# Kernel optimization log

Measured on AMD Instinct MI355X. Metric: run time of the kernel, lower is better.

The kernel has to match this reference:

```python
import jax, jax.numpy as jnp
import numpy as np

B, CIN, COUT, H, W, WDIM = 16, 256, 256, 64, 64, 512


def setup_inputs() -> dict:
    key = jax.random.key(0)
    ks = jax.random.split(key, 4)
    return {
        "x": jax.random.normal(ks[0], (B, CIN, H, W), dtype=jnp.float32),
        "w": jax.random.normal(ks[1], (B, WDIM), dtype=jnp.float32),
        "affine_w": jax.random.normal(ks[2], (CIN, WDIM), dtype=jnp.float32),
        "affine_b": jnp.ones((CIN,), dtype=jnp.float32),
        "weight": jax.random.normal(ks[3], (COUT, CIN, 1, 1), dtype=jnp.float32),
        "bias": jnp.zeros((COUT,), dtype=jnp.float32),
    }


def reference(x, w, affine_w, affine_b, weight, bias):
    # Affine: FullyConnectedLayer with weight_gain = 1/sqrt(w_dim), bias_init=1
    wg = 1.0 / np.sqrt(WDIM).astype(np.float32)
    styles = w @ (affine_w.T * wg) + affine_b  # [B, CIN]

    # Pre-normalize weight and styles (demodulate branch)
    wk = weight[:, :, 0, 0]  # [COUT, CIN] (1x1 kernel)
    wk = wk * jax.lax.rsqrt(jnp.mean(jnp.square(weight), axis=(1, 2, 3)))[:, None]
    s = styles * jax.lax.rsqrt(jnp.mean(jnp.square(styles)))  # [B, CIN]

    # Per-sample modulated weights: [B, COUT, CIN]
    wb = wk[None, :, :] * s[:, None, :]
    dcoef = jax.lax.rsqrt(jnp.sum(jnp.square(wb), axis=2) + 1e-8)  # [B, COUT]
    wb = wb * dcoef[:, :, None]

    # Grouped 1x1 conv == batched GEMM over spatial positions
    y = jnp.einsum('bihw,boi->bohw', x, wb) + bias[None, :, None, None]

    # Bilinear upsample x2 (align_corners=False == half-pixel, jax default)
    y = jax.image.resize(y, (B, COUT, 2 * H, 2 * W), method='bilinear')
    return y
```

## Files before the change

### kernel.cpp

```cpp
#include <hip/hip_runtime.h>
#include <hip/hip_bf16.h>

#define B_   16
#define CIN  256
#define COUT 256
#define HH   64
#define WW   64
#define WDIM 512
#define OH   128
#define OW   128

typedef __attribute__((ext_vector_type(8))) short short8;
typedef __attribute__((ext_vector_type(4))) float f32x4;

__device__ __forceinline__ unsigned short f2bf(float f) {
    __hip_bfloat16 h = __float2bfloat16(f);
    return *reinterpret_cast<unsigned short*>(&h);
}
__device__ __forceinline__ float bf2f(unsigned short u) {
    unsigned int t = ((unsigned int)u) << 16;
    return *reinterpret_cast<float*>(&t);
}


__global__ __launch_bounds__(256) void k_styles(const float* __restrict__ w,
                                                const float* __restrict__ aw,
                                                const float* __restrict__ ab,
                                                float* __restrict__ ws) {
    int b = blockIdx.x, i = threadIdx.x;
    const float4* wr = (const float4*)(w + b * WDIM);
    const float4* ar = (const float4*)(aw + (size_t)i * WDIM);
    float acc = 0.f;
    #pragma unroll 4
    for (int k = 0; k < WDIM / 4; ++k) {
        float4 wv = wr[k], av = ar[k];
        acc += wv.x * av.x + wv.y * av.y + wv.z * av.z + wv.w * av.w;
    }
    const float wg = 0.04419417382415922f;
    float st = acc * wg + ab[i];
    ws[64 + b * CIN + i] = st;
    __shared__ float sred[256];
    sred[i] = st * st;
    __syncthreads();
    for (int s = 128; s > 0; s >>= 1) {
        if (i < s) sred[i] += sred[i + s];
        __syncthreads();
    }
    if (i == 0) ws[b] = sred[0];
}

__global__ __launch_bounds__(64) void k_wb(const float* __restrict__ weight,
                                           const float* __restrict__ ws,
                                           unsigned short* __restrict__ wb) {
    int o = blockIdx.x, b = blockIdx.y, l = threadIdx.x;
    float tot = 0.f;
    #pragma unroll
    for (int j = 0; j < B_; ++j) tot += ws[j];
    float srs = rsqrtf(tot / (float)(B_ * CIN));
    float4 wk = *(const float4*)(weight + (size_t)o * CIN + l * 4);
    float ss = wk.x * wk.x + wk.y * wk.y + wk.z * wk.z + wk.w * wk.w;
    #pragma unroll
    for (int off = 32; off; off >>= 1) ss += __shfl_xor(ss, off);
    float wkn = rsqrtf(ss / (float)CIN);
    float4 st = *(const float4*)(ws + 64 + b * CIN + l * 4);
    float4 t;
    t.x = wk.x * wkn * st.x * srs;
    t.y = wk.y * wkn * st.y * srs;
    t.z = wk.z * wkn * st.z * srs;
    t.w = wk.w * wkn * st.w * srs;
    float s2 = t.x * t.x + t.y * t.y + t.z * t.z + t.w * t.w;
    #pragma unroll
    for (int off = 32; off; off >>= 1) s2 += __shfl_xor(s2, off);
    float dcoef = rsqrtf(s2 + 1e-8f);
    ushort4 pk;
    pk.x = f2bf(t.x * dcoef);
    pk.y = f2bf(t.y * dcoef);
    pk.z = f2bf(t.z * dcoef);
    pk.w = f2bf(t.w * dcoef);
    *(ushort4*)(wb + ((size_t)b * COUT + o) * CIN + l * 4) = pk;
}

__global__ __launch_bounds__(512, 4) void k_conv5(const float* __restrict__ x,
                                                  const float* __restrict__ bias,
                                                  const unsigned short* __restrict__ wb,
                                                  unsigned short* __restrict__ y) {
    __shared__ __align__(16) unsigned short xt[128 * CIN];
    const int r2 = blockIdx.x * 2;
    const int b = blockIdx.y;
    const int tid = threadIdx.x;
    const int lane = tid & 63;
    const int wv = tid >> 6;
    const int lo = lane & 15, hi = lane >> 4;

    const unsigned short* wbb = wb + (size_t)b * COUT * CIN;
    short8 breg[2][8];
    #pragma unroll
    for (int c = 0; c < 2; ++c) {
        const int m0 = (wv * 2 + c) * 16;
        const unsigned short* wrow = wbb + (size_t)(m0 + lo) * CIN + hi * 8;
        #pragma unroll
        for (int ks = 0; ks < 8; ++ks)
            breg[c][ks] = *(const short8*)(wrow + ks * 32);
    }

    {
        const int c4 = tid & 15;
        const int rowsel = (tid >> 4) & 1;
        const int ig = tid >> 5;
        const float* xp = x + (size_t)b * CIN * (HH * WW) + (size_t)(r2 + rowsel) * WW + c4 * 4;
        const int pxbase = rowsel * 64 + c4 * 4;
        #pragma unroll
        for (int p = 0; p < 8; ++p) {
            const int i0 = ig * 16 + p * 2;
            float4 v0 = *(const float4*)(xp + (size_t)i0 * (HH * WW));
            float4 v1 = *(const float4*)(xp + (size_t)(i0 + 1) * (HH * WW));
            const int ib = i0 >> 3, e = i0 & 7;
            #pragma unroll
            for (int j = 0; j < 4; ++j) {
                const int px = pxbase + j;
                float f0 = (j == 0) ? v0.x : (j == 1) ? v0.y : (j == 2) ? v0.z : v0.w;
                float f1 = (j == 0) ? v1.x : (j == 1) ? v1.y : (j == 2) ? v1.z : v1.w;
                unsigned int pk = (unsigned int)f2bf(f0) | ((unsigned int)f2bf(f1) << 16);
                const int swz = ib ^ (px & 31) ^ ((px >> 2) & 7);
                *(unsigned int*)&xt[px * 256 + (swz << 3) + e] = pk;
            }
        }
    }
    __syncthreads();

    unsigned short* yb = y + (size_t)b * COUT * (HH * WW);

    #pragma unroll
    for (int c = 0; c < 2; ++c) {
        const int m0 = (wv * 2 + c) * 16;
        const float bs = bias[m0 + lo];
        unsigned short* yrow = yb + (size_t)(m0 + lo) * (HH * WW);
        #pragma unroll
        for (int g = 0; g < 8; ++g) {
            f32x4 acc = {0.f, 0.f, 0.f, 0.f};
            #pragma unroll
            for (int ks = 0; ks < 8; ++ks) {
                const int px = g * 16 + lo;
                const int ib = ks * 4 + hi;
                const int swz = ib ^ (px & 31) ^ ((px >> 2) & 7);
                short8 a = *(const short8*)&xt[px * 256 + (swz << 3)];
                acc = __builtin_amdgcn_mfma_f32_16x16x32_bf16(a, breg[c][ks], acc, 0, 0, 0);
            }
            ushort4 pk;
            pk.x = f2bf(acc[0] + bs);
            pk.y = f2bf(acc[1] + bs);
            pk.z = f2bf(acc[2] + bs);
            pk.w = f2bf(acc[3] + bs);
            const int prow = g >> 2;
            const int pcol = (g & 3) * 16 + hi * 4;
            *(ushort4*)(yrow + (size_t)(r2 + prow) * WW + pcol) = pk;
        }
    }
}

__global__ __launch_bounds__(256, 8) void k_up(const unsigned short* __restrict__ y,
                                               float* __restrict__ out) {
    const int tid = threadIdx.x;
    const int t = tid & 31;
    const int s = tid >> 5;
    const int idx = blockIdx.x * 8 + s;
    const int p = idx & 63;
    const int ch = (idx >> 6) & 255;
    const int b = idx >> 14;

    const unsigned short* yb = y + (size_t)(b * COUT + ch) * (HH * WW);
    const int pm1 = max(p - 1, 0), pp1 = min(p + 1, HH - 1);
    unsigned int T  = *(const unsigned int*)(yb + pm1 * WW + 2 * t);
    unsigned int M  = *(const unsigned int*)(yb + p   * WW + 2 * t);
    unsigned int Bt = *(const unsigned int*)(yb + pp1 * WW + 2 * t);

    float tB = bf2f((unsigned short)(T & 0xffff)),  tC = bf2f((unsigned short)(T >> 16));
    float mB = bf2f((unsigned short)(M & 0xffff)),  mC = bf2f((unsigned short)(M >> 16));
    float bB = bf2f((unsigned short)(Bt & 0xffff)), bC = bf2f((unsigned short)(Bt >> 16));

    float aB = 0.25f * tB + 0.75f * mB, aC = 0.25f * tC + 0.75f * mC;
    float eB = 0.75f * mB + 0.25f * bB, eC = 0.75f * mC + 0.25f * bC;

    float aA = __shfl_up(aC, 1, 32);   if (t == 0)  aA = aB;
    float aD = __shfl_down(aB, 1, 32); if (t == 31) aD = aC;
    float eA = __shfl_up(eC, 1, 32);   if (t == 0)  eA = eB;
    float eD = __shfl_down(eB, 1, 32); if (t == 31) eD = eC;

    float4 o0, o1;
    o0.x = 0.25f * aA + 0.75f * aB;
    o0.y = 0.75f * aB + 0.25f * aC;
    o0.z = 0.25f * aB + 0.75f * aC;
    o0.w = 0.75f * aC + 0.25f * aD;
    o1.x = 0.25f * eA + 0.75f * eB;
    o1.y = 0.75f * eB + 0.25f * eC;
    o1.z = 0.25f * eB + 0.75f * eC;
    o1.w = 0.75f * eC + 0.25f * eD;

    float* op = out + (size_t)(b * COUT + ch) * (OH * OW) + (2 * p) * OW + 4 * t;
    *(float4*)op = o0;
    *(float4*)(op + OW) = o1;
}

extern "C" void kernel_launch(void* const* d_in, const int* in_sizes, int n_in,
                              void* d_out, int out_size, void* d_ws, size_t ws_size,
                              hipStream_t stream) {
    (void)in_sizes; (void)n_in; (void)out_size; (void)ws_size;
    const float* x      = (const float*)d_in[0];
    const float* w      = (const float*)d_in[1];
    const float* aw     = (const float*)d_in[2];
    const float* ab     = (const float*)d_in[3];
    const float* weight = (const float*)d_in[4];
    const float* bias   = (const float*)d_in[5];
    float* out = (float*)d_out;
    float* wsf = (float*)d_ws;
    unsigned short* wb = (unsigned short*)((char*)d_ws + 32768);
    unsigned short* y  = (unsigned short*)((char*)d_ws + (4u << 20));

    hipLaunchKernelGGL(k_styles, dim3(16), dim3(256), 0, stream, w, aw, ab, wsf);
    hipLaunchKernelGGL(k_wb, dim3(COUT, B_), dim3(64), 0, stream, weight, wsf, wb);
    hipLaunchKernelGGL(k_conv5, dim3(HH / 2, B_), dim3(512), 0, stream, x, bias, wb, y);
    hipLaunchKernelGGL(k_up, dim3(B_ * COUT * HH / 8), dim3(256), 0, stream, y, out);
}
```

Measured before the change: 111.3 us.

## Fuse 1x1 modulated conv with bilinear upsample using LDS-resident conv output

Merges the conv kernel and the upsample kernel into one kernel. Each block now computes conv output for two adjacent input rows (with halo overlap) into shared memory and writes the upsampled float output directly. This removes the bf16 intermediate write and read through global memory and one kernel launch. In exchange, x loads and conv MFMA work are doubled because neighbouring blocks overlap by one row. LDS use roughly doubles, which lowers occupancy. The second weight register set is also loaded after the barrier to ease register pressure.

Measured after the change: 120.4 us. +8.2%, slower.

```diff
diff --git a/kernel.cpp b/kernel.cpp
--- a/kernel.cpp
+++ b/kernel.cpp
@@ -80,12 +80,13 @@
     *(ushort4*)(wb + ((size_t)b * COUT + o) * CIN + l * 4) = pk;
 }
 
-__global__ __launch_bounds__(512, 4) void k_conv5(const float* __restrict__ x,
+__global__ __launch_bounds__(512, 2) void k_fused(const float* __restrict__ x,
                                                   const float* __restrict__ bias,
                                                   const unsigned short* __restrict__ wb,
-                                                  unsigned short* __restrict__ y) {
+                                                  float* __restrict__ out) {
     __shared__ __align__(16) unsigned short xt[128 * CIN];
-    const int r2 = blockIdx.x * 2;
+    __shared__ __align__(16) unsigned int yl[COUT * 64];
+    const int r = blockIdx.x;
     const int b = blockIdx.y;
     const int tid = threadIdx.x;
     const int lane = tid & 63;
@@ -93,21 +94,21 @@
     const int lo = lane & 15, hi = lane >> 4;
 
     const unsigned short* wbb = wb + (size_t)b * COUT * CIN;
-    short8 breg[2][8];
-    #pragma unroll
-    for (int c = 0; c < 2; ++c) {
-        const int m0 = (wv * 2 + c) * 16;
-        const unsigned short* wrow = wbb + (size_t)(m0 + lo) * CIN + hi * 8;
-        #pragma unroll
-        for (int ks = 0; ks < 8; ++ks)
-            breg[c][ks] = *(const short8*)(wrow + ks * 32);
+    const int m0_0 = (wv * 2 + 0) * 16;
+    const int m0_1 = (wv * 2 + 1) * 16;
+    short8 breg0[8], breg1[8];
+    {
+        const unsigned short* wrow = wbb + (size_t)(m0_0 + lo) * CIN + hi * 8;
+        #pragma unroll
+        for (int ks = 0; ks < 8; ++ks) breg0[ks] = *(const short8*)(wrow + ks * 32);
     }
 
     {
         const int c4 = tid & 15;
         const int rowsel = (tid >> 4) & 1;
         const int ig = tid >> 5;
-        const float* xp = x + (size_t)b * CIN * (HH * WW) + (size_t)(r2 + rowsel) * WW + c4 * 4;
+        const int grow = min(r + rowsel, HH - 1);
+        const float* xp = x + (size_t)b * CIN * (HH * WW) + (size_t)grow * WW + c4 * 4;
         const int pxbase = rowsel * 64 + c4 * 4;
         #pragma unroll
         for (int p = 0; p < 8; ++p) {
@@ -128,13 +129,19 @@
     }
     __syncthreads();
 
-    unsigned short* yb = y + (size_t)b * COUT * (HH * WW);
+    {
+        const unsigned short* wrow = wbb + (size_t)(m0_1 + lo) * CIN + hi * 8;
+        #pragma unroll
+        for (int ks = 0; ks < 8; ++ks) breg1[ks] = *(const short8*)(wrow + ks * 32);
+    }
 
     #pragma unroll
     for (int c = 0; c < 2; ++c) {
-        const int m0 = (wv * 2 + c) * 16;
-        const float bs = bias[m0 + lo];
-        unsigned short* yrow = yb + (size_t)(m0 + lo) * (HH * WW);
+        const int m0 = c ? m0_1 : m0_0;
+        const int o = m0 + lo;
+        const float bs = bias[o];
+        const int rot = 2 * (o & 15);
+        unsigned int* yrow = &yl[o * 64];
         #pragma unroll
         for (int g = 0; g < 8; ++g) {
             f32x4 acc = {0.f, 0.f, 0.f, 0.f};
@@ -144,61 +151,53 @@
                 const int ib = ks * 4 + hi;
                 const int swz = ib ^ (px & 31) ^ ((px >> 2) & 7);
                 short8 a = *(const short8*)&xt[px * 256 + (swz << 3)];
-                acc = __builtin_amdgcn_mfma_f32_16x16x32_bf16(a, breg[c][ks], acc, 0, 0, 0);
+                acc = __builtin_amdgcn_mfma_f32_16x16x32_bf16(
+                        a, c ? breg1[ks] : breg0[ks], acc, 0, 0, 0);
             }
-            ushort4 pk;
-            pk.x = f2bf(acc[0] + bs);
-            pk.y = f2bf(acc[1] + bs);
-            pk.z = f2bf(acc[2] + bs);
-            pk.w = f2bf(acc[3] + bs);
-            const int prow = g >> 2;
-            const int pcol = (g & 3) * 16 + hi * 4;
-            *(ushort4*)(yrow + (size_t)(r2 + prow) * WW + pcol) = pk;
+            const int p2 = g * 8 + hi * 2;
+            unsigned int u0 = (unsigned int)f2bf(acc[0] + bs) | ((unsigned int)f2bf(acc[1] + bs) << 16);
+            unsigned int u1 = (unsigned int)f2bf(acc[2] + bs) | ((unsigned int)f2bf(acc[3] + bs) << 16);
+            const int cc = (p2 + rot) & 63;
+            yrow[cc] = u0;
+            yrow[cc + 1] = u1;
         }
     }
-}
-
-__global__ __launch_bounds__(256, 8) void k_up(const unsigned short* __restrict__ y,
-                                               float* __restrict__ out) {
-    const int tid = threadIdx.x;
+    __syncthreads();
+
+    const int ostart = (r == 0) ? 0 : (2 * r + 1);
+    const int nrows = (r == 0) ? 3 : ((r == HH - 1) ? 1 : 2);
+    const int iters = nrows * 16;
+    const int h = tid >> 5;
     const int t = tid & 31;
-    const int s = tid >> 5;
-    const int idx = blockIdx.x * 8 + s;
-    const int p = idx & 63;
-    const int ch = (idx >> 6) & 255;
-    const int b = idx >> 14;
-
-    const unsigned short* yb = y + (size_t)(b * COUT + ch) * (HH * WW);
-    const int pm1 = max(p - 1, 0), pp1 = min(p + 1, HH - 1);
-    unsigned int T  = *(const unsigned int*)(yb + pm1 * WW + 2 * t);
-    unsigned int M  = *(const unsigned int*)(yb + p   * WW + 2 * t);
-    unsigned int Bt = *(const unsigned int*)(yb + pp1 * WW + 2 * t);
-
-    float tB = bf2f((unsigned short)(T & 0xffff)),  tC = bf2f((unsigned short)(T >> 16));
-    float mB = bf2f((unsigned short)(M & 0xffff)),  mC = bf2f((unsigned short)(M >> 16));
-    float bB = bf2f((unsigned short)(Bt & 0xffff)), bC = bf2f((unsigned short)(Bt >> 16));
-
-    float aB = 0.25f * tB + 0.75f * mB, aC = 0.25f * tC + 0.75f * mC;
-    float eB = 0.75f * mB + 0.25f * bB, eC = 0.75f * mC + 0.25f * bC;
-
-    float aA = __shfl_up(aC, 1, 32);   if (t == 0)  aA = aB;
-    float aD = __shfl_down(aB, 1, 32); if (t == 31) aD = aC;
-    float eA = __shfl_up(eC, 1, 32);   if (t == 0)  eA = eB;
-    float eD = __shfl_down(eB, 1, 32); if (t == 31) eD = eC;
-
-    float4 o0, o1;
-    o0.x = 0.25f * aA + 0.75f * aB;
-    o0.y = 0.75f * aB + 0.25f * aC;
-    o0.z = 0.25f * aB + 0.75f * aC;
-    o0.w = 0.75f * aC + 0.25f * aD;
-    o1.x = 0.25f * eA + 0.75f * eB;
-    o1.y = 0.75f * eB + 0.25f * eC;
-    o1.z = 0.25f * eB + 0.75f * eC;
-    o1.w = 0.75f * eC + 0.25f * eD;
-
-    float* op = out + (size_t)(b * COUT + ch) * (OH * OW) + (2 * p) * OW + 4 * t;
-    *(float4*)op = o0;
-    *(float4*)(op + OW) = o1;
+
+    for (int i = 0; i < iters; ++i) {
+        const int task = i * 16 + h;
+        const int o = task & 255;
+        const int ori = task >> 8;
+        const int orow = ostart + ori;
+        const int yr0 = (orow - 1) >> 1;
+        const int lr0 = min(max(yr0, 0), HH - 1) - r;
+        const int lr1 = min(yr0 + 1, HH - 1) - r;
+        const float wr0 = (orow & 1) ? 0.75f : 0.25f;
+        const float wr1 = 1.f - wr0;
+        const int rot = 2 * (o & 15);
+        const unsigned int* yrow = &yl[o * 64];
+        unsigned int M0 = yrow[(lr0 * 32 + t + rot) & 63];
+        unsigned int M1 = yrow[(lr1 * 32 + t + rot) & 63];
+        float mB = bf2f((unsigned short)(M0 & 0xffff)), mC = bf2f((unsigned short)(M0 >> 16));
+        float nB = bf2f((unsigned short)(M1 & 0xffff)), nC = bf2f((unsigned short)(M1 >> 16));
+        float vB = wr0 * mB + wr1 * nB;
+        float vC = wr0 * mC + wr1 * nC;
+        float vA = __shfl_up(vC, 1, 32);   if (t == 0)  vA = vB;
+        float vD = __shfl_down(vB, 1, 32); if (t == 31) vD = vC;
+        float4 ov;
+        ov.x = 0.25f * vA + 0.75f * vB;
+        ov.y = 0.75f * vB + 0.25f * vC;
+        ov.z = 0.25f * vB + 0.75f * vC;
+        ov.w = 0.75f * vC + 0.25f * vD;
+        float* op = out + (((size_t)(b * COUT + o) * OH) + orow) * OW + 4 * t;
+        *(float4*)op = ov;
+    }
 }
 
 extern "C" void kernel_launch(void* const* d_in, const int* in_sizes, int n_in,
@@ -214,10 +213,8 @@
     float* out = (float*)d_out;
     float* wsf = (float*)d_ws;
     unsigned short* wb = (unsigned short*)((char*)d_ws + 32768);
-    unsigned short* y  = (unsigned short*)((char*)d_ws + (4u << 20));
 
     hipLaunchKernelGGL(k_styles, dim3(16), dim3(256), 0, stream, w, aw, ab, wsf);
     hipLaunchKernelGGL(k_wb, dim3(COUT, B_), dim3(64), 0, stream, weight, wsf, wb);
-    hipLaunchKernelGGL(k_conv5, dim3(HH / 2, B_), dim3(512), 0, stream, x, bias, wb, y);
-    hipLaunchKernelGGL(k_up, dim3(B_ * COUT * HH / 8), dim3(256), 0, stream, y, out);
-}
+    hipLaunchKernelGGL(k_fused, dim3(HH, B_), dim3(512), 0, stream, x, bias, wb, out);
+}
```
